# Performance work log

Measured on AMD Instinct MI355X. Metric: run time of the kernel, lower is better.

## Reference

```python
import jax, jax.numpy as jnp
import numpy as np

B, L, ENC_D, DEC_D, ATTN_D = 64, 1024, 512, 512, 512


def setup_inputs() -> dict:
    key = jax.random.key(0)
    ks = jax.random.split(key, 8)
    s_enc = 1.0 / np.sqrt(ENC_D)
    s_dec = 1.0 / np.sqrt(DEC_D)
    s_att = 1.0 / np.sqrt(ATTN_D)
    return {
        "enc_out": jax.random.normal(ks[0], (B, L, ENC_D), dtype=jnp.float32),
        "dec_hidden": jax.random.normal(ks[1], (B, DEC_D), dtype=jnp.float32),
        # nn.Linear params (uniform(-1/sqrt(fan_in), 1/sqrt(fan_in)))
        "W_enc": jax.random.uniform(ks[2], (ENC_D, ATTN_D), jnp.float32, -s_enc, s_enc),
        "b_enc": jax.random.uniform(ks[3], (ATTN_D,), jnp.float32, -s_enc, s_enc),
        "W_dec": jax.random.uniform(ks[4], (DEC_D, ATTN_D), jnp.float32, -s_dec, s_dec),
        "b_dec": jax.random.uniform(ks[5], (ATTN_D,), jnp.float32, -s_dec, s_dec),
        "W_full": jax.random.uniform(ks[6], (ATTN_D,), jnp.float32, -s_att, s_att),
        "b_full": jax.random.uniform(ks[7], (), jnp.float32, -s_att, s_att),
    }


def reference(enc_out, dec_hidden, W_enc, b_enc, W_dec, b_dec, W_full, b_full):
    # attn1: [B, L, A]; attn2: [B, A]
    attn1 = jnp.einsum("ble,ea->bla", enc_out, W_enc) + b_enc
    attn2 = dec_hidden @ W_dec + b_dec
    # full_attn(relu(attn1 + attn2[:, None])) -> [B, L]
    attn = jnp.einsum("bla,a->bl", jax.nn.relu(attn1 + attn2[:, None, :]), W_full) + b_full
    alpha = jax.nn.softmax(attn, axis=1)  # over L
    attn_weighted_enc = jnp.einsum("ble,bl->be", enc_out, alpha)
    return attn_weighted_enc, alpha
```

## Files before the change

kernel.cpp:

```cpp
#include <hip/hip_runtime.h>
#include <hip/hip_bf16.h>

typedef __bf16 bf16x8 __attribute__((ext_vector_type(8)));
typedef float f32x4 __attribute__((ext_vector_type(4)));
typedef unsigned int u32;

#define WS_WT     0
#define WS_BIAS   524288
#define WS_LOGITS 655360
#define WS_PART   917504

__device__ __forceinline__ unsigned short f2bf(float f) {
    __bf16 h = (__bf16)f;
    return __builtin_bit_cast(unsigned short, h);
}

__device__ __forceinline__ void gload_lds16(const void* g, void* l) {
    __builtin_amdgcn_global_load_lds(
        (const __attribute__((address_space(1))) u32*)g,
        (__attribute__((address_space(3))) u32*)l, 16, 0, 0);
}

__global__ void k_wt(const float* __restrict__ W, unsigned short* __restrict__ Wt) {
    int n = blockIdx.x;
    for (int k = threadIdx.x; k < 512; k += 256)
        Wt[n * 512 + k] = f2bf(W[k * 512 + n]);
}

__global__ void k_bias2(const float* __restrict__ dec, const float* __restrict__ Wd,
                        const float* __restrict__ b_dec, const float* __restrict__ b_enc,
                        float* __restrict__ bias2p) {
    int blk = blockIdx.x;
    int b = blk >> 2, nc = blk & 3;
    int t = threadIdx.x;
    __shared__ float sdec[512];
    __shared__ float red[256];
    for (int k = t; k < 512; k += 256) sdec[k] = dec[b * 512 + k];
    __syncthreads();
    int n = nc * 128 + (t & 127);
    int kh = t >> 7;
    float acc = 0.f;
    int k0 = kh * 256;
    #pragma unroll 4
    for (int k = k0; k < k0 + 256; ++k)
        acc += sdec[k] * Wd[k * 512 + n];
    red[t] = acc;
    __syncthreads();
    if (t < 128) {
        int nn = nc * 128 + t;
        bias2p[b * 512 + nn] = red[t] + red[t + 128] + b_dec[nn] + b_enc[nn];
    }
}

__global__ __launch_bounds__(256, 4) void k_logits(
        const float* __restrict__ enc, const unsigned short* __restrict__ Wt,
        const float* __restrict__ bias2p, const float* __restrict__ Wf,
        float* __restrict__ logits) {
    __shared__ __align__(16) unsigned short lds[2][8192];
    __shared__ f32x4 comb[2][2][64];

    int t = threadIdx.x;
    int lane = t & 63;
    int w = t >> 6;
    int rg = w >> 1;
    int h = w & 1;
    int blk = blockIdx.x;
    int b = blk >> 4;
    int m = lane & 15;
    int g = lane >> 4;

    #define STAGE(bufi, nc_)                                                      \
        {                                                                         \
            int n0_ = (nc_) * 16;                                                 \
            _Pragma("unroll")                                                     \
            for (int j = 0; j < 4; ++j) {                                         \
                int c_ = w * 4 + j;                                               \
                const char* src_ = (const char*)Wt + (size_t)(n0_ + c_) * 1024    \
                                   + ((lane ^ c_) << 4);                          \
                gload_lds16(src_, (char*)&lds[bufi][0] + c_ * 1024);              \
            }                                                                     \
        }

    STAGE(0, 0)

    bf16x8 A0[8], A1[8];
    {
        const float* ap0 = enc + (size_t)(blk * 64 + rg * 32 + m) * 512 + h * 256 + g * 8;
        const float* ap1 = ap0 + 16 * 512;
        #pragma unroll
        for (int f = 0; f < 8; ++f) {
            float4 x = *(const float4*)(ap0 + f * 32);
            float4 y = *(const float4*)(ap0 + f * 32 + 4);
            bf16x8 a;
            a[0] = (__bf16)x.x; a[1] = (__bf16)x.y; a[2] = (__bf16)x.z; a[3] = (__bf16)x.w;
            a[4] = (__bf16)y.x; a[5] = (__bf16)y.y; a[6] = (__bf16)y.z; a[7] = (__bf16)y.w;
            A0[f] = a;
            float4 x1 = *(const float4*)(ap1 + f * 32);
            float4 y1 = *(const float4*)(ap1 + f * 32 + 4);
            bf16x8 a1;
            a1[0] = (__bf16)x1.x; a1[1] = (__bf16)x1.y; a1[2] = (__bf16)x1.z; a1[3] = (__bf16)x1.w;
            a1[4] = (__bf16)y1.x; a1[5] = (__bf16)y1.y; a1[6] = (__bf16)y1.z; a1[7] = (__bf16)y1.w;
            A1[f] = a1;
        }
    }
    #pragma unroll
    for (int f = 0; f < 8; ++f)
        asm volatile("" : "+v"(A0[f]), "+v"(A1[f]));

    __syncthreads();

    float p[4] = {0.f, 0.f, 0.f, 0.f};
    int swz = m << 4;

    for (int nc = 0; nc < 32; ++nc) {
        int buf = nc & 1;
        if (nc < 31) {
            if (buf) STAGE(0, nc + 1) else STAGE(1, nc + 1)
        }
        const char* base = (const char*)&lds[buf][0] + m * 1024;
        f32x4 acc0 = {0.f, 0.f, 0.f, 0.f};
        f32x4 acc1 = {0.f, 0.f, 0.f, 0.f};
        #pragma unroll
        for (int f = 0; f < 8; ++f) {
            uint4 raw = *(const uint4*)(base + (((h * 8 + f) * 64 + g * 16) ^ swz));
            bf16x8 bfr = __builtin_bit_cast(bf16x8, raw);
            acc0 = __builtin_amdgcn_mfma_f32_16x16x32_bf16(A0[f], bfr, acc0, 0, 0, 0);
            acc1 = __builtin_amdgcn_mfma_f32_16x16x32_bf16(A1[f], bfr, acc1, 0, 0, 0);
        }
        comb[rg][h ^ 1][lane] = h ? acc0 : acc1;
        __syncthreads();
        f32x4 other = comb[rg][h][lane];
        f32x4 own = h ? acc1 : acc0;
        int col = nc * 16 + m;
        float bias = bias2p[b * 512 + col];
        float wf = Wf[col];
        #pragma unroll
        for (int r = 0; r < 4; ++r) {
            float v = own[r] + other[r] + bias;
            v = v > 0.f ? v : 0.f;
            p[r] += v * wf;
        }
        __syncthreads();
    }

    #pragma unroll
    for (int r = 0; r < 4; ++r) {
        float v = p[r];
        v += __shfl_xor(v, 1, 64);
        v += __shfl_xor(v, 2, 64);
        v += __shfl_xor(v, 4, 64);
        v += __shfl_xor(v, 8, 64);
        if (m == 0) logits[blk * 64 + rg * 32 + h * 16 + g * 4 + r] = v;
    }
}

__global__ void k_softmax(const float* __restrict__ logits, float* __restrict__ alpha) {
    int b = blockIdx.x;
    int t = threadIdx.x;
    __shared__ float red[256];
    float4 v = ((const float4*)(logits + b * 1024))[t];
    float mx = fmaxf(fmaxf(v.x, v.y), fmaxf(v.z, v.w));
    red[t] = mx;
    __syncthreads();
    for (int s = 128; s > 0; s >>= 1) {
        if (t < s) red[t] = fmaxf(red[t], red[t + s]);
        __syncthreads();
    }
    mx = red[0];
    __syncthreads();
    float4 e;
    e.x = expf(v.x - mx); e.y = expf(v.y - mx);
    e.z = expf(v.z - mx); e.w = expf(v.w - mx);
    red[t] = e.x + e.y + e.z + e.w;
    __syncthreads();
    for (int s = 128; s > 0; s >>= 1) {
        if (t < s) red[t] += red[t + s];
        __syncthreads();
    }
    float inv = 1.0f / red[0];
    float4 o;
    o.x = e.x * inv; o.y = e.y * inv; o.z = e.z * inv; o.w = e.w * inv;
    ((float4*)(alpha + b * 1024))[t] = o;
}

__global__ void k_wsum_part(const float* __restrict__ enc, const float* __restrict__ alpha,
                            float* __restrict__ part) {
    int blk = blockIdx.x;
    int b = blk >> 3, c = blk & 7;
    int t = threadIdx.x;
    int col = (t & 127) * 4;
    int lh = t >> 7;
    const float* ep = enc + (size_t)(b * 1024 + c * 128) * 512;
    const float* al = alpha + b * 1024 + c * 128;
    float4 s = {0.f, 0.f, 0.f, 0.f};
    #pragma unroll 4
    for (int i = 0; i < 64; ++i) {
        int l = i * 2 + lh;
        float a = al[l];
        float4 e = *(const float4*)(ep + (size_t)l * 512 + col);
        s.x += e.x * a; s.y += e.y * a; s.z += e.z * a; s.w += e.w * a;
    }
    __shared__ float red[2][512];
    *(float4*)&red[lh][col] = s;
    __syncthreads();
    if (t < 128) {
        float4 a0 = *(const float4*)&red[0][t * 4];
        float4 a1 = *(const float4*)&red[1][t * 4];
        float4 o;
        o.x = a0.x + a1.x; o.y = a0.y + a1.y;
        o.z = a0.z + a1.z; o.w = a0.w + a1.w;
        *(float4*)(part + (size_t)blk * 512 + t * 4) = o;
    }
}

__global__ void k_wsum_final(const float* __restrict__ part, float* __restrict__ out) {
    int b = blockIdx.x;
    int t = threadIdx.x;
    float4 s = {0.f, 0.f, 0.f, 0.f};
    #pragma unroll
    for (int c = 0; c < 8; ++c) {
        float4 v = *(const float4*)(part + (size_t)(b * 8 + c) * 512 + t * 4);
        s.x += v.x; s.y += v.y; s.z += v.z; s.w += v.w;
    }
    *(float4*)(out + b * 512 + t * 4) = s;
}

extern "C" void kernel_launch(void* const* d_in, const int* in_sizes, int n_in,
                              void* d_out, int out_size, void* d_ws, size_t ws_size,
                              hipStream_t stream) {
    const float* enc    = (const float*)d_in[0];
    const float* dec    = (const float*)d_in[1];
    const float* W_enc  = (const float*)d_in[2];
    const float* b_enc  = (const float*)d_in[3];
    const float* W_dec  = (const float*)d_in[4];
    const float* b_dec  = (const float*)d_in[5];
    const float* W_full = (const float*)d_in[6];

    float* out = (float*)d_out;
    char* ws = (char*)d_ws;
    unsigned short* Wt = (unsigned short*)(ws + WS_WT);
    float* bias2p = (float*)(ws + WS_BIAS);
    float* logits = (float*)(ws + WS_LOGITS);
    float* part   = (float*)(ws + WS_PART);
    float* alpha  = out + 32768;

    hipLaunchKernelGGL(k_wt,         dim3(512),  dim3(256), 0, stream, W_enc, Wt);
    hipLaunchKernelGGL(k_bias2,      dim3(256),  dim3(256), 0, stream, dec, W_dec, b_dec, b_enc, bias2p);
    hipLaunchKernelGGL(k_logits,     dim3(1024), dim3(256), 0, stream, enc, Wt, bias2p, W_full, logits);
    hipLaunchKernelGGL(k_softmax,    dim3(64),   dim3(256), 0, stream, logits, alpha);
    hipLaunchKernelGGL(k_wsum_part,  dim3(512),  dim3(256), 0, stream, enc, alpha, part);
    hipLaunchKernelGGL(k_wsum_final, dim3(64),   dim3(128), 0, stream, part, out);
}
```

Measured before the change: 110.5 us.

## Switch logits GEMM to 32x32 MFMA with pre-fragmented weights read from global

Weights are now pre-arranged by k_wt into the exact MFMA B-fragment order. k_logits gives each wave a full 32-row tile with all of K held in registers and uses 32x32x16 MFMAs. B fragments are loaded straight from global/L2 instead of being staged through LDS, which removes the LDS double buffering, the cross-wave combine and both __syncthreads per chunk. The cost is heavy register pressure: 32 bf16x8 A fragments plus 16 accumulators force occupancy down to 2 blocks per CU. Every wave also re-reads the whole weight matrix from cache.

```diff
diff --git a/kernel.cpp b/kernel.cpp
--- a/kernel.cpp
+++ b/kernel.cpp
@@ -3,6 +3,7 @@
 
 typedef __bf16 bf16x8 __attribute__((ext_vector_type(8)));
 typedef float f32x4 __attribute__((ext_vector_type(4)));
+typedef float f32x16 __attribute__((ext_vector_type(16)));
 typedef unsigned int u32;
 
 #define WS_WT     0
@@ -15,16 +16,19 @@
     return __builtin_bit_cast(unsigned short, h);
 }
 
-__device__ __forceinline__ void gload_lds16(const void* g, void* l) {
-    __builtin_amdgcn_global_load_lds(
-        (const __attribute__((address_space(1))) u32*)g,
-        (__attribute__((address_space(3))) u32*)l, 16, 0, 0);
-}
-
-__global__ void k_wt(const float* __restrict__ W, unsigned short* __restrict__ Wt) {
-    int n = blockIdx.x;
-    for (int k = threadIdx.x; k < 512; k += 256)
-        Wt[n * 512 + k] = f2bf(W[k * 512 + n]);
+__global__ void k_wt(const float* __restrict__ W, unsigned short* __restrict__ WtF) {
+    int u = (blockIdx.x * 256 + threadIdx.x) * 4;
+    #pragma unroll
+    for (int i = 0; i < 4; ++i) {
+        int idx = u + i;
+        int e = idx & 7;
+        int l = (idx >> 3) & 63;
+        int f = (idx >> 9) & 31;
+        int nc = idx >> 14;
+        int n = nc * 32 + (l & 31);
+        int k = f * 16 + (l >> 5) * 8 + e;
+        WtF[idx] = f2bf(W[k * 512 + n]);
+    }
 }
 
 __global__ void k_bias2(const float* __restrict__ dec, const float* __restrict__ Wd,
@@ -52,105 +56,78 @@
     }
 }
 
-__global__ __launch_bounds__(256, 4) void k_logits(
-        const float* __restrict__ enc, const unsigned short* __restrict__ Wt,
+__global__ __launch_bounds__(256, 2) void k_logits(
+        const float* __restrict__ enc, const unsigned short* __restrict__ WtF,
         const float* __restrict__ bias2p, const float* __restrict__ Wf,
         float* __restrict__ logits) {
-    __shared__ __align__(16) unsigned short lds[2][8192];
-    __shared__ f32x4 comb[2][2][64];
-
     int t = threadIdx.x;
     int lane = t & 63;
     int w = t >> 6;
-    int rg = w >> 1;
-    int h = w & 1;
     int blk = blockIdx.x;
-    int b = blk >> 4;
-    int m = lane & 15;
-    int g = lane >> 4;
-
-    #define STAGE(bufi, nc_)                                                      \
-        {                                                                         \
-            int n0_ = (nc_) * 16;                                                 \
-            _Pragma("unroll")                                                     \
-            for (int j = 0; j < 4; ++j) {                                         \
-                int c_ = w * 4 + j;                                               \
-                const char* src_ = (const char*)Wt + (size_t)(n0_ + c_) * 1024    \
-                                   + ((lane ^ c_) << 4);                          \
-                gload_lds16(src_, (char*)&lds[bufi][0] + c_ * 1024);              \
-            }                                                                     \
-        }
-
-    STAGE(0, 0)
-
-    bf16x8 A0[8], A1[8];
+    int row0 = blk * 128 + w * 32;
+    int b = blk >> 3;
+    int cl = lane & 31;
+    int hf = lane >> 5;
+
+    bf16x8 A[32];
     {
-        const float* ap0 = enc + (size_t)(blk * 64 + rg * 32 + m) * 512 + h * 256 + g * 8;
-        const float* ap1 = ap0 + 16 * 512;
+        const float* ap = enc + (size_t)(row0 + cl) * 512 + hf * 8;
         #pragma unroll
-        for (int f = 0; f < 8; ++f) {
-            float4 x = *(const float4*)(ap0 + f * 32);
-            float4 y = *(const float4*)(ap0 + f * 32 + 4);
+        for (int f = 0; f < 32; ++f) {
+            float4 x = *(const float4*)(ap + f * 16);
+            float4 y = *(const float4*)(ap + f * 16 + 4);
             bf16x8 a;
             a[0] = (__bf16)x.x; a[1] = (__bf16)x.y; a[2] = (__bf16)x.z; a[3] = (__bf16)x.w;
             a[4] = (__bf16)y.x; a[5] = (__bf16)y.y; a[6] = (__bf16)y.z; a[7] = (__bf16)y.w;
-            A0[f] = a;
-            float4 x1 = *(const float4*)(ap1 + f * 32);
-            float4 y1 = *(const float4*)(ap1 + f * 32 + 4);
-            bf16x8 a1;
-            a1[0] = (__bf16)x1.x; a1[1] = (__bf16)x1.y; a1[2] = (__bf16)x1.z; a1[3] = (__bf16)x1.w;
-            a1[4] = (__bf16)y1.x; a1[5] = (__bf16)y1.y; a1[6] = (__bf16)y1.z; a1[7] = (__bf16)y1.w;
-            A1[f] = a1;
+            A[f] = a;
         }
     }
     #pragma unroll
-    for (int f = 0; f < 8; ++f)
-        asm volatile("" : "+v"(A0[f]), "+v"(A1[f]));
-
-    __syncthreads();
-
-    float p[4] = {0.f, 0.f, 0.f, 0.f};
-    int swz = m << 4;
-
-    for (int nc = 0; nc < 32; ++nc) {
-        int buf = nc & 1;
-        if (nc < 31) {
-            if (buf) STAGE(0, nc + 1) else STAGE(1, nc + 1)
+    for (int f = 0; f < 32; ++f)
+        asm volatile("" : "+v"(A[f]));
+
+    float p[16];
+    #pragma unroll
+    for (int r = 0; r < 16; ++r) p[r] = 0.f;
+
+    const uint4* bbase = (const uint4*)WtF + lane;
+
+    for (int nc = 0; nc < 16; ++nc) {
+        const uint4* bp = bbase + nc * 2048;
+        f32x16 acc = {};
+        #pragma unroll
+        for (int gq = 0; gq < 4; ++gq) {
+            uint4 raw[8];
+            #pragma unroll
+            for (int j = 0; j < 8; ++j)
+                raw[j] = bp[(gq * 8 + j) * 64];
+            #pragma unroll
+            for (int j = 0; j < 8; ++j) {
+                bf16x8 bfr = __builtin_bit_cast(bf16x8, raw[j]);
+                acc = __builtin_amdgcn_mfma_f32_32x32x16_bf16(A[gq * 8 + j], bfr, acc, 0, 0, 0);
+            }
         }
-        const char* base = (const char*)&lds[buf][0] + m * 1024;
-        f32x4 acc0 = {0.f, 0.f, 0.f, 0.f};
-        f32x4 acc1 = {0.f, 0.f, 0.f, 0.f};
-        #pragma unroll
-        for (int f = 0; f < 8; ++f) {
-            uint4 raw = *(const uint4*)(base + (((h * 8 + f) * 64 + g * 16) ^ swz));
-            bf16x8 bfr = __builtin_bit_cast(bf16x8, raw);
-            acc0 = __builtin_amdgcn_mfma_f32_16x16x32_bf16(A0[f], bfr, acc0, 0, 0, 0);
-            acc1 = __builtin_amdgcn_mfma_f32_16x16x32_bf16(A1[f], bfr, acc1, 0, 0, 0);
-        }
-        comb[rg][h ^ 1][lane] = h ? acc0 : acc1;
-        __syncthreads();
-        f32x4 other = comb[rg][h][lane];
-        f32x4 own = h ? acc1 : acc0;
-        int col = nc * 16 + m;
+        int col = nc * 32 + cl;
         float bias = bias2p[b * 512 + col];
         float wf = Wf[col];
         #pragma unroll
-        for (int r = 0; r < 4; ++r) {
-            float v = own[r] + other[r] + bias;
+        for (int r = 0; r < 16; ++r) {
+            float v = acc[r] + bias;
             v = v > 0.f ? v : 0.f;
             p[r] += v * wf;
         }
-        __syncthreads();
-    }
-
-    #pragma unroll
-    for (int r = 0; r < 4; ++r) {
+    }
+
+    #pragma unroll
+    for (int r = 0; r < 16; ++r) {
         float v = p[r];
         v += __shfl_xor(v, 1, 64);
         v += __shfl_xor(v, 2, 64);
         v += __shfl_xor(v, 4, 64);
         v += __shfl_xor(v, 8, 64);
-        if (m == 0) logits[blk * 64 + rg * 32 + h * 16 + g * 4 + r] = v;
+        v += __shfl_xor(v, 16, 64);
+        if (cl == 0)
+            logits[row0 + (r & 3) + 8 * (r >> 2) + 4 * hf] = v;
     }
 }
 
@@ -238,15 +215,15 @@
 
     float* out = (float*)d_out;
     char* ws = (char*)d_ws;
-    unsigned short* Wt = (unsigned short*)(ws + WS_WT);
+    unsigned short* WtF = (unsigned short*)(ws + WS_WT);
     float* bias2p = (float*)(ws + WS_BIAS);
     float* logits = (float*)(ws + WS_LOGITS);
     float* part   = (float*)(ws + WS_PART);
     float* alpha  = out + 32768;
 
-    hipLaunchKernelGGL(k_wt,         dim3(512),  dim3(256), 0, stream, W_enc, Wt);
+    hipLaunchKernelGGL(k_wt,         dim3(256),  dim3(256), 0, stream, W_enc, WtF);
     hipLaunchKernelGGL(k_bias2,      dim3(256),  dim3(256), 0, stream, dec, W_dec, b_dec, b_enc, bias2p);
-    hipLaunchKernelGGL(k_logits,     dim3(1024), dim3(256), 0, stream, enc, Wt, bias2p, W_full, logits);
+    hipLaunchKernelGGL(k_logits,     dim3(512),  dim3(256), 0, stream, enc, WtF, bias2p, W_full, logits);
     hipLaunchKernelGGL(k_softmax,    dim3(64),   dim3(256), 0, stream, logits, alpha);
     hipLaunchKernelGGL(k_wsum_part,  dim3(512),  dim3(256), 0, stream, enc, alpha, part);
     hipLaunchKernelGGL(k_wsum_final, dim3(64),   dim3(128), 0, stream, part, out);
```

Measured after the change: 143.4 us. 1.3x slower.
